# Optimization experiments

Measured on AMD Instinct MI355X. Metric: run time of the kernel, lower is better.

The kernel has to match this reference:

```python
import jax, jax.numpy as jnp
import numpy as np
from jax import lax


def _dct_basis():
    # 64 separable 2D DCT-II basis filters, shape [64,1,8,8] (OIHW)
    k = 8
    a = np.full(k, np.sqrt(2.0 / k)); a[0] = np.sqrt(1.0 / k)
    u = np.arange(k)[:, None]; xx = np.arange(k)[None, :]
    B = a[:, None] * np.cos((2 * xx + 1) * u * np.pi / (2 * k))  # [u, x]
    basis = np.einsum('ux,vy->uvxy', B, B).reshape(64, 1, k, k)
    return jnp.asarray(basis, dtype=jnp.float32)


def _conv(x, w, b, pad):
    y = lax.conv_general_dilated(x, w, (1, 1), [(pad, pad), (pad, pad)],
                                 dimension_numbers=('NCHW', 'OIHW', 'NCHW'))
    return y + b[None, :, None, None]


def _bn(x, s, b, m, v, eps=1e-5):
    inv = s * lax.rsqrt(v + eps)
    return x * inv[None, :, None, None] + (b - m * inv)[None, :, None, None]


def _mp2(x):
    return lax.reduce_window(x, -jnp.inf, lax.max, (1, 1, 2, 2), (1, 1, 2, 2), 'VALID')


def setup_inputs() -> dict:
    key = jax.random.key(0)
    ks = jax.random.split(key, 32)
    B = 128
    d = {}
    d['x'] = jax.random.normal(ks[0], (B, 1, 256, 256), jnp.float32)
    d['qvectors'] = jax.random.uniform(ks[1], (B, 64), jnp.float32)
    d['dct_basis'] = _dct_basis()
    def w(k, shape, sc=0.02):
        return jax.random.normal(k, shape, jnp.float32) * sc
    # conv stack
    d['conv1a_w'] = w(ks[2], (64, 1, 5, 5));   d['conv1a_b'] = w(ks[3], (64,))
    d['conv1b_w'] = w(ks[4], (64, 64, 5, 5));  d['conv1b_b'] = w(ks[5], (64,))
    d['conv2a_w'] = w(ks[6], (128, 64, 5, 5)); d['conv2a_b'] = w(ks[7], (128,))
    d['conv3a_w'] = w(ks[8], (256, 128, 5, 5)); d['conv3a_b'] = w(ks[9], (256,))
    # batchnorm (eval-mode) params: scale, bias, running_mean, running_var
    for i, (name, c) in enumerate([('bn1a', 64), ('bn1b', 64), ('bn2a', 128), ('bn3a', 256)]):
        kk = jax.random.split(ks[10 + i], 4)
        d[name + '_s'] = 1.0 + w(kk[0], (c,))
        d[name + '_b'] = w(kk[1], (c,))
        d[name + '_m'] = w(kk[2], (c,))
        d[name + '_v'] = jax.random.uniform(kk[3], (c,), jnp.float32, 0.5, 1.5)
    d['fc1_w'] = w(ks[20], (500, 15 * 8 * 256 + 64), 0.01); d['fc1_b'] = w(ks[21], (500,))
    d['fc2_w'] = w(ks[22], (500, 564), 0.01);               d['fc2_b'] = w(ks[23], (500,))
    d['fc3_w'] = w(ks[24], (2, 564), 0.01);                 d['fc3_b'] = w(ks[25], (2,))
    return d


def reference(x, qvectors, dct_basis,
              conv1a_w, conv1a_b, bn1a_s, bn1a_b, bn1a_m, bn1a_v,
              conv1b_w, conv1b_b, bn1b_s, bn1b_b, bn1b_m, bn1b_v,
              conv2a_w, conv2a_b, bn2a_s, bn2a_b, bn2a_m, bn2a_v,
              conv3a_w, conv3a_b, bn3a_s, bn3a_b, bn3a_m, bn3a_v,
              fc1_w, fc1_b, fc2_w, fc2_b, fc3_w, fc3_b):
    gamma = 1e6
    # --- soft-histogram over DCT coefficients (no_grad in the original) ---
    dct = lax.conv_general_dilated(x, dct_basis, (8, 8), 'VALID',
                                   dimension_numbers=('NCHW', 'OIHW', 'NCHW'))  # [B,64,32,32]
    bins = jnp.arange(-60, 61, dtype=jnp.float32)  # 121 bins

    def step(_, b):
        s = jnp.sum(jax.nn.sigmoid(gamma * (dct - b)), axis=(2, 3)) / 1024.0  # [B,64]
        return None, s
    _, feats = lax.scan(step, None, bins)           # [121,B,64]
    feats = jnp.transpose(feats, (1, 0, 2))          # [B,121,64]
    features = feats[:, 0:120, :] - feats[:, 1:121, :]
    features = lax.stop_gradient(features.reshape(-1, 1, 120, 64))

    # --- CNN backbone ---
    h = jax.nn.relu(_bn(_conv(features, conv1a_w, conv1a_b, 2), bn1a_s, bn1a_b, bn1a_m, bn1a_v))
    h = jax.nn.relu(_bn(_conv(h, conv1b_w, conv1b_b, 2), bn1b_s, bn1b_b, bn1b_m, bn1b_v))
    h = _mp2(h)
    h = jax.nn.relu(_bn(_conv(h, conv2a_w, conv2a_b, 2), bn2a_s, bn2a_b, bn2a_m, bn2a_v))
    h = _mp2(h)
    h = jax.nn.relu(_bn(_conv(h, conv3a_w, conv3a_b, 2), bn3a_s, bn3a_b, bn3a_m, bn3a_v))
    h = _mp2(h)                                      # [B,256,15,8]
    h_flat = h.reshape(-1, 15 * 8 * 256)
    h = jnp.concatenate([qvectors, h_flat], axis=1)
    h = jax.nn.relu(h @ fc1_w.T + fc1_b)
    h = jnp.concatenate([qvectors, h], axis=1)
    h = jax.nn.relu(h @ fc2_w.T + fc2_b)
    h = jnp.concatenate([qvectors, h], axis=1)
    return h @ fc3_w.T + fc3_b
```

## Files before the change

### kernel.cpp

```cpp
#include <hip/hip_runtime.h>


typedef _Float16 half8 __attribute__((ext_vector_type(8)));
typedef _Float16 half4 __attribute__((ext_vector_type(4)));
typedef float f32x16 __attribute__((ext_vector_type(16)));

__device__ __forceinline__ void async_copy16(const void* g, void* l) {
  __builtin_amdgcn_global_load_lds(
      (__attribute__((address_space(1))) void*)g,
      (__attribute__((address_space(3))) void*)l, 16, 0, 0);
}

__global__ __launch_bounds__(256) void dct_kernel(const float* __restrict__ x,
                                                  const float* __restrict__ basis,
                                                  float* __restrict__ dct) {
  __shared__ __align__(16) float Bm[64];
  int tid = threadIdx.x;
  if (tid < 64) {
    int u = tid >> 3, xx = tid & 7;
    Bm[tid] = basis[(u * 8) * 64 + xx * 8] * 2.8284271247461903f;
  }
  __syncthreads();
  int gid = blockIdx.x * 256 + tid;
  int b = gid >> 10, blk = gid & 1023;
  int bi = blk >> 5, bj = blk & 31;
  const float* xp = x + (size_t)b * 65536 + (bi * 8) * 256 + bj * 8;
  float X[64];
#pragma unroll
  for (int r = 0; r < 8; ++r) {
    float4 p = *(const float4*)(xp + r * 256);
    float4 q = *(const float4*)(xp + r * 256 + 4);
    X[r * 8 + 0] = p.x; X[r * 8 + 1] = p.y; X[r * 8 + 2] = p.z; X[r * 8 + 3] = p.w;
    X[r * 8 + 4] = q.x; X[r * 8 + 5] = q.y; X[r * 8 + 6] = q.z; X[r * 8 + 7] = q.w;
  }
  float T[64];
#pragma unroll
  for (int u = 0; u < 8; ++u) {
    float t[8] = {0.f, 0.f, 0.f, 0.f, 0.f, 0.f, 0.f, 0.f};
#pragma unroll
    for (int xx = 0; xx < 8; ++xx) {
      float bm = Bm[u * 8 + xx];
#pragma unroll
      for (int y = 0; y < 8; ++y) t[y] += bm * X[xx * 8 + y];
    }
#pragma unroll
    for (int y = 0; y < 8; ++y) T[u * 8 + y] = t[y];
  }
  float* op = dct + (size_t)b * 65536 + bi * 32 + bj;
#pragma unroll
  for (int v = 0; v < 8; ++v) {
    float dc[8] = {0.f, 0.f, 0.f, 0.f, 0.f, 0.f, 0.f, 0.f};
#pragma unroll
    for (int y = 0; y < 8; ++y) {
      float bm = Bm[v * 8 + y];
#pragma unroll
      for (int u = 0; u < 8; ++u) dc[u] += bm * T[u * 8 + y];
    }
#pragma unroll
    for (int u = 0; u < 8; ++u) op[(u * 8 + v) * 1024] = dc[u];
  }
}

__global__ __launch_bounds__(256) void hist_kernel(const float* __restrict__ dct,
                                                   float* __restrict__ feat) {
  __shared__ __align__(16) float h[16 * 121];
  int tid = threadIdx.x;
  for (int i = tid; i < 16 * 121; i += 256) h[i] = 0.f;
  __syncthreads();
  int b = blockIdx.x >> 6, c = blockIdx.x & 63;
  const float* dp = dct + (size_t)(b * 64 + c) * 1024;
  float* hc = h + (tid & 15) * 121;
  float4 v4 = ((const float4*)dp)[tid];
  float vals[4] = {v4.x, v4.y, v4.z, v4.w};
#pragma unroll
  for (int i = 0; i < 4; ++i) {
    float d = vals[i];
    float fl = floorf(d);
    float t0 = d - fl;
    int k = (int)fl + 60;
    if (t0 >= 2e-5f && t0 <= 1.f - 1.2e-4f) {
      if (k >= 0 && k < 120) atomicAdd(hc + k, 1.0f);
    } else {
      float s0 = 1.f / (1.f + expf(-1e6f * t0));
      float s1 = 1.f / (1.f + expf(1e6f * (1.f - t0)));
      if (k >= 1 && k <= 120) atomicAdd(hc + k - 1, 1.f - s0);
      if (k >= 0 && k < 120)  atomicAdd(hc + k, s0 - s1);
      if (k >= -1 && k < 119) atomicAdd(hc + k + 1, s1);
    }
  }
  __syncthreads();
  for (int f = tid; f < 120; f += 256) {
    float s = 0.f;
#pragma unroll
    for (int l = 0; l < 16; ++l) s += h[l * 121 + f];
    feat[((size_t)b * 120 + f) * 64 + c] = s * (1.f / 1024.f);
  }
}

template <int CI, int CO>
__global__ __launch_bounds__(256) void wtrans(const float* __restrict__ w,
                                              _Float16* __restrict__ wt) {
  int i = blockIdx.x * 256 + threadIdx.x;
  if (i >= (CI / 8) * 30 * CO * 8) return;
  int c8 = i & 7;
  int t = i >> 3;
  int co = t % CO; t /= CO;
  int k = t % 30;
  int cg = t / 30;
  int ci = cg * 8 + c8;
  int kh = k / 6, kw = k % 6;
  float v = (kw < 5) ? w[((size_t)co * CI + ci) * 25 + kh * 5 + kw] : 0.f;
  wt[i] = (_Float16)v;
}

__global__ __launch_bounds__(256) void bnprep(const float* __restrict__ cb,
                                              const float* __restrict__ s,
                                              const float* __restrict__ b,
                                              const float* __restrict__ m,
                                              const float* __restrict__ v,
                                              float* __restrict__ scale,
                                              float* __restrict__ shift, int n) {
  int i = threadIdx.x;
  if (i < n) {
    float inv = s[i] * rsqrtf(v[i] + 1e-5f);
    scale[i] = inv;
    shift[i] = (cb[i] - m[i]) * inv + b[i];
  }
}

__global__ __launch_bounds__(256) void conv1a_f16(
    const float* __restrict__ in, const float* __restrict__ wts,
    const float* __restrict__ cb, const float* __restrict__ s_,
    const float* __restrict__ b_, const float* __restrict__ m_,
    const float* __restrict__ v_, _Float16* __restrict__ out) {
  __shared__ __align__(16) float wl[5 * 8 * 20];
  __shared__ __align__(16) float il[12 * 68];
  int tid = threadIdx.x, bid = blockIdx.x;
  int img = bid / 30;
  int r = bid % 30;
  int cob = r / 15;
  int h0 = (r % 15) * 8;
  int cog = tid & 7, wg = (tid >> 3) & 3, hh = tid >> 5;
  float acc[4][16];
#pragma unroll
  for (int i = 0; i < 4; ++i)
#pragma unroll
    for (int j = 0; j < 16; ++j) acc[i][j] = 0.f;
  for (int idx = tid; idx < 32 * 25; idx += 256) {
    int rr = idx % 25, co = idx / 25;
    float v = wts[(cob * 32 + co) * 25 + rr];
    int kh = rr / 5, kw = rr % 5;
    wl[(kh * 8 + (co >> 2)) * 20 + (co & 3) * 5 + kw] = v;
  }
  for (int idx = tid; idx < 12 * 68; idx += 256) {
    int cc = idx % 68, rr = idx / 68;
    int hy = h0 + rr - 2, wx = cc - 2;
    float v = 0.f;
    if (hy >= 0 && hy < 120 && wx >= 0 && wx < 64)
      v = in[(size_t)img * 7680 + hy * 64 + wx];
    il[idx] = v;
  }
  __syncthreads();
#pragma unroll
  for (int kh = 0; kh < 5; ++kh) {
    const float* ir = &il[(hh + kh) * 68 + wg * 16];
    float iv[20];
#pragma unroll
    for (int i = 0; i < 5; ++i) {
      float4 p = *(const float4*)(ir + i * 4);
      iv[i * 4] = p.x; iv[i * 4 + 1] = p.y; iv[i * 4 + 2] = p.z; iv[i * 4 + 3] = p.w;
    }
    const float* wr = &wl[(kh * 8 + cog) * 20];
    float wv[20];
#pragma unroll
    for (int i = 0; i < 5; ++i) {
      float4 p = *(const float4*)(wr + i * 4);
      wv[i * 4] = p.x; wv[i * 4 + 1] = p.y; wv[i * 4 + 2] = p.z; wv[i * 4 + 3] = p.w;
    }
#pragma unroll
    for (int co = 0; co < 4; ++co)
#pragma unroll
      for (int kw = 0; kw < 5; ++kw) {
        float w1 = wv[co * 5 + kw];
#pragma unroll
        for (int w = 0; w < 16; ++w) acc[co][w] += w1 * iv[w + kw];
      }
  }
  int h = h0 + hh;
  int co0 = cob * 32 + cog * 4;
  float inv[4], bia[4];
#pragma unroll
  for (int i = 0; i < 4; ++i) {
    int c = co0 + i;
    inv[i] = s_[c] * rsqrtf(v_[c] + 1e-5f);
    bia[i] = (cb[c] - m_[c]) * inv[i] + b_[c];
  }
  int g = co0 >> 3, off = co0 & 7;
  _Float16* op = out + (((size_t)(img * 8 + g) * 120 + h) * 64) * 8 + off;
#pragma unroll
  for (int w = 0; w < 16; ++w) {
    half4 o;
#pragma unroll
    for (int i = 0; i < 4; ++i)
      o[i] = (_Float16)fmaxf(acc[i][w] * inv[i] + bia[i], 0.f);
    *(half4*)&op[(size_t)(wg * 16 + w) * 8] = o;
  }
}

template <int CI, int CO, int H, int W, int BLK_M, bool OUT_NCHW>
__global__ __launch_bounds__(256, 2) void conv5_mfma(
    const _Float16* __restrict__ in, const _Float16* __restrict__ wt,
    const float* __restrict__ scale, const float* __restrict__ shift,
    _Float16* __restrict__ out) {
  constexpr int NW_M = BLK_M / 64;
  constexpr int NW_N = 4 / NW_M;
  constexpr int BLK_N = NW_N * 128;
  constexpr int ROWS = BLK_N / W;
  constexpr int TB = (H + ROWS - 1) / ROWS;
  constexpr int NCOB = CO / BLK_M;
  constexpr int HR = ROWS + 4;
  constexpr int HC = W + 4;
  constexpr int CIG = CI / 8;
  constexpr int AITER = (HR * HC + 255) / 256;
  constexpr int WBYTES = 30 * BLK_M * 16;
  constexpr int WITER = (WBYTES + 4095) / 4096;
  __shared__ __align__(16) _Float16 Alds[HR * HC * 8 + 8];
  __shared__ __align__(16) _Float16 Wlds[30 * BLK_M * 8];

  int tid = threadIdx.x;
  int bid = blockIdx.x;
  int img = bid / (TB * NCOB);
  int r = bid % (TB * NCOB);
  int tb = r / NCOB;
  int cob = r % NCOB;
  int h0 = tb * ROWS;

  int wid = tid >> 6, l = tid & 63, lo = l & 31, hi = l >> 5;
  int widM = wid / NW_N, widN = wid % NW_N;

  if (tid < 8) Alds[HR * HC * 8 + tid] = (_Float16)0.f;

  int wbase[2];
#pragma unroll
  for (int mi = 0; mi < 2; ++mi)
    wbase[mi] = (hi * BLK_M + widM * 64 + mi * 32 + lo) * 8;
  int bbase[4], pr_[4], pc_[4];
#pragma unroll
  for (int j = 0; j < 4; ++j) {
    int pix = widN * 128 + j * 32 + lo;
    pr_[j] = pix / W;
    pc_[j] = pix % W;
    bbase[j] = (pr_[j] * HC + pc_[j] + hi) * 8;
  }

  f32x16 acc[2][4];
#pragma unroll
  for (int mi = 0; mi < 2; ++mi)
#pragma unroll
    for (int j = 0; j < 4; ++j) acc[mi][j] = (f32x16){};

#pragma unroll 1
  for (int ci0 = 0; ci0 < CI; ci0 += 8) {
    int cg = ci0 >> 3;
    const _Float16* ing = in + (size_t)(img * CIG + cg) * H * W * 8;
    half8 areg[AITER];
#pragma unroll
    for (int it = 0; it < AITER; ++it) {
      int i = tid + it * 256;
      half8 v = {};
      if (i < HR * HC) {
        int rr = i / HC, cc = i % HC;
        int hy = h0 + rr - 2, wx = cc - 2;
        if (hy >= 0 && hy < H && wx >= 0 && wx < W)
          v = *(const half8*)&ing[(size_t)(hy * W + wx) * 8];
      }
      areg[it] = v;
    }
    const char* wsrc = (const char*)(wt + ((size_t)cg * 30 * CO + cob * BLK_M) * 8);
#pragma unroll
    for (int rr = 0; rr < WITER; ++rr) {
      int f = rr * 4096 + tid * 16;
      if (f < WBYTES) {
        int row = f / (BLK_M * 16);
        int off = f % (BLK_M * 16);
        async_copy16(wsrc + (size_t)row * (CO * 16) + off,
                     (char*)Wlds + (rr * 4096 + wid * 1024));
      }
    }
#pragma unroll
    for (int it = 0; it < AITER; ++it) {
      int i = tid + it * 256;
      if (i < HR * HC) *(half8*)&Alds[i * 8] = areg[it];
    }
    __syncthreads();
#pragma unroll
    for (int kh = 0; kh < 5; ++kh) {
#pragma unroll
      for (int kwb = 0; kwb < 3; ++kwb) {
        half8 af[2], bf[4];
#pragma unroll
        for (int mi = 0; mi < 2; ++mi)
          af[mi] = *(const half8*)&Wlds[wbase[mi] + (kh * 6 + 2 * kwb) * BLK_M * 8];
#pragma unroll
        for (int j = 0; j < 4; ++j)
          bf[j] = *(const half8*)&Alds[bbase[j] + (kh * HC + 2 * kwb) * 8];
#pragma unroll
        for (int mi = 0; mi < 2; ++mi)
#pragma unroll
          for (int j = 0; j < 4; ++j)
            acc[mi][j] = __builtin_amdgcn_mfma_f32_32x32x16_f16(
                af[mi], bf[j], acc[mi][j], 0, 0, 0);
      }
    }
    __syncthreads();
  }

  if (!OUT_NCHW) {
    constexpr int CGO = CO / 8;
    int gbase = (cob * BLK_M + widM * 64) >> 3;
#pragma unroll
    for (int mi = 0; mi < 2; ++mi) {
#pragma unroll
      for (int r4 = 0; r4 < 4; ++r4) {
        int g = gbase + mi * 4 + r4;
        int co0 = g * 8 + hi * 4;
        float4 sv = *(const float4*)&scale[co0];
        float4 tv = *(const float4*)&shift[co0];
#pragma unroll
        for (int j = 0; j < 4; ++j) {
          int hy = h0 + pr_[j];
          if (hy < H) {
            half4 o;
            o[0] = (_Float16)fmaxf(acc[mi][j][r4 * 4 + 0] * sv.x + tv.x, 0.f);
            o[1] = (_Float16)fmaxf(acc[mi][j][r4 * 4 + 1] * sv.y + tv.y, 0.f);
            o[2] = (_Float16)fmaxf(acc[mi][j][r4 * 4 + 2] * sv.z + tv.z, 0.f);
            o[3] = (_Float16)fmaxf(acc[mi][j][r4 * 4 + 3] * sv.w + tv.w, 0.f);
            *(half4*)&out[(((size_t)(img * CGO + g) * H + hy) * W + pc_[j]) * 8 +
                          hi * 4] = o;
          }
        }
      }
    }
  } else {
#pragma unroll
    for (int mi = 0; mi < 2; ++mi) {
#pragma unroll
      for (int reg = 0; reg < 16; ++reg) {
        int co = cob * BLK_M + widM * 64 + mi * 32 + (reg & 3) + 8 * (reg >> 2) + 4 * hi;
        float s = scale[co], t = shift[co];
#pragma unroll
        for (int j = 0; j < 4; ++j) {
          int hy = h0 + pr_[j];
          if (hy < H)
            out[((size_t)(img * CO + co) * H + hy) * W + pc_[j]] =
                (_Float16)fmaxf(acc[mi][j][reg] * s + t, 0.f);
        }
      }
    }
  }
}

template <int IMGS, int CG, int H, int W>
__global__ __launch_bounds__(256) void pool_g(const _Float16* __restrict__ in,
                                              _Float16* __restrict__ out) {
  constexpr int OH = H / 2, OW = W / 2;
  int idx = blockIdx.x * 256 + threadIdx.x;
  constexpr int TOTAL = IMGS * CG * OH * OW;
  if (idx >= TOTAL) return;
  int ow = idx % OW;
  int t = idx / OW;
  int oh = t % OH; t /= OH;
  int g = t % CG;
  int img = t / CG;
  const half8* in8 = (const half8*)in;
  size_t base = ((size_t)(img * CG + g) * H + 2 * oh) * W + 2 * ow;
  half8 a = in8[base], b = in8[base + 1], c = in8[base + W], d = in8[base + W + 1];
  half8 o;
#pragma unroll
  for (int i = 0; i < 8; ++i) {
    _Float16 m0 = a[i] > b[i] ? a[i] : b[i];
    _Float16 m1 = c[i] > d[i] ? c[i] : d[i];
    o[i] = m0 > m1 ? m0 : m1;
  }
  ((half8*)out)[((size_t)(img * CG + g) * OH + oh) * OW + ow] = o;
}

__global__ __launch_bounds__(256) void pool_nchw(const _Float16* __restrict__ in,
                                                 _Float16* __restrict__ out) {
  int idx = blockIdx.x * 256 + threadIdx.x;
  if (idx >= 128 * 256 * 15) return;
  int oh = idx % 15;
  int t = idx / 15;
  int c = t % 256;
  int img = t / 256;
  const half8* r = (const half8*)(in + ((size_t)(img * 256 + c) * 30 + 2 * oh) * 16);
  half8 x0 = r[0], x1 = r[1], y0 = r[2], y1 = r[3];
  half8 o;
#pragma unroll
  for (int ow = 0; ow < 4; ++ow) {
    _Float16 m0 = x0[2 * ow] > x0[2 * ow + 1] ? x0[2 * ow] : x0[2 * ow + 1];
    _Float16 m1 = y0[2 * ow] > y0[2 * ow + 1] ? y0[2 * ow] : y0[2 * ow + 1];
    o[ow] = m0 > m1 ? m0 : m1;
    _Float16 n0 = x1[2 * ow] > x1[2 * ow + 1] ? x1[2 * ow] : x1[2 * ow + 1];
    _Float16 n1 = y1[2 * ow] > y1[2 * ow + 1] ? y1[2 * ow] : y1[2 * ow + 1];
    o[ow + 4] = n0 > n1 ? n0 : n1;
  }
  ((half8*)out)[((size_t)(img * 256 + c) * 15 + oh)] = o;
}

__global__ __launch_bounds__(256, 2) void fc1_mfma(const float* __restrict__ qv,
                                                   const _Float16* __restrict__ p3,
                                                   const float* __restrict__ w,
                                                   float* __restrict__ part) {
  __shared__ __align__(16) _Float16 Wl[8 * 256 * 8];
  __shared__ __align__(16) _Float16 Bl[8 * 128 * 8];
  int tid = threadIdx.x;
  int ks = blockIdx.x >> 1, mt = blockIdx.x & 1;
  int wid = tid >> 6, l = tid & 63, lo = l & 31, hi = l >> 5;
  f32x16 acc[2][4];
#pragma unroll
  for (int mi = 0; mi < 2; ++mi)
#pragma unroll
    for (int j = 0; j < 4; ++j) acc[mi][j] = (f32x16){};

#pragma unroll 1
  for (int i3 = 0; i3 < 3; ++i3) {
    int c = ks + 240 * i3;
    if (c > 480) break;
    for (int idx = tid; idx < 2048; idx += 256) {
      int n_loc = idx >> 3, k8 = idx & 7;
      int n = mt * 256 + n_loc;
      half8 v = {};
      if (n < 500) {
        const float* src = w + (size_t)n * 30784 + c * 64 + k8 * 8;
        float4 f0 = *(const float4*)src;
        float4 f1 = *(const float4*)(src + 4);
        v[0] = (_Float16)f0.x; v[1] = (_Float16)f0.y;
        v[2] = (_Float16)f0.z; v[3] = (_Float16)f0.w;
        v[4] = (_Float16)f1.x; v[5] = (_Float16)f1.y;
        v[6] = (_Float16)f1.z; v[7] = (_Float16)f1.w;
      }
      *(half8*)&Wl[(size_t)(k8 * 256 + n_loc) * 8] = v;
    }
    for (int idx = tid; idx < 1024; idx += 256) {
      int img = idx >> 3, k8 = idx & 7;
      half8 v;
      if (c == 0) {
        const float* src = qv + img * 64 + k8 * 8;
        float4 f0 = *(const float4*)src;
        float4 f1 = *(const float4*)(src + 4);
        v[0] = (_Float16)f0.x; v[1] = (_Float16)f0.y;
        v[2] = (_Float16)f0.z; v[3] = (_Float16)f0.w;
        v[4] = (_Float16)f1.x; v[5] = (_Float16)f1.y;
        v[6] = (_Float16)f1.z; v[7] = (_Float16)f1.w;
      } else {
        v = *(const half8*)&p3[(size_t)img * 30720 + (c * 64 - 64) + k8 * 8];
      }
      *(half8*)&Bl[(size_t)(k8 * 128 + img) * 8] = v;
    }
    __syncthreads();
#pragma unroll
    for (int ks16 = 0; ks16 < 4; ++ks16) {
      half8 af[2], bf[4];
#pragma unroll
      for (int mi = 0; mi < 2; ++mi)
        af[mi] = *(const half8*)&Wl[(size_t)((ks16 * 2 + hi) * 256 + wid * 64 +
                                             mi * 32 + lo) * 8];
#pragma unroll
      for (int j = 0; j < 4; ++j)
        bf[j] = *(const half8*)&Bl[(size_t)((ks16 * 2 + hi) * 128 + j * 32 + lo) * 8];
#pragma unroll
      for (int mi = 0; mi < 2; ++mi)
#pragma unroll
        for (int j = 0; j < 4; ++j)
          acc[mi][j] = __builtin_amdgcn_mfma_f32_32x32x16_f16(
              af[mi], bf[j], acc[mi][j], 0, 0, 0);
    }
    __syncthreads();
  }
#pragma unroll
  for (int mi = 0; mi < 2; ++mi)
#pragma unroll
    for (int reg = 0; reg < 16; ++reg) {
      int n = mt * 256 + wid * 64 + mi * 32 + (reg & 3) + 8 * (reg >> 2) + 4 * hi;
#pragma unroll
      for (int j = 0; j < 4; ++j)
        part[((size_t)ks * 512 + n) * 128 + j * 32 + lo] = acc[mi][j][reg];
    }
}

__global__ __launch_bounds__(256) void fc1_reduce(const float* __restrict__ part,
                                                  const float* __restrict__ bias,
                                                  float* __restrict__ out) {
  int idx = blockIdx.x * 256 + threadIdx.x;
  int img = idx & 127, n = idx >> 7;
  float s = 0.f;
#pragma unroll 8
  for (int ks = 0; ks < 240; ++ks) s += part[((size_t)ks * 512 + n) * 128 + img];
  out[n * 128 + img] = (n < 500) ? fmaxf(s + bias[n], 0.f) : 0.f;
}

__global__ __launch_bounds__(256) void fc2_kernel(const float* __restrict__ qv,
                                                  const float* __restrict__ fc1o,
                                                  const float* __restrict__ w,
                                                  const float* __restrict__ bias,
                                                  float* __restrict__ out) {
  int idx = blockIdx.x * 256 + threadIdx.x;
  if (idx >= 128 * 500) return;
  int m = idx & 127, n = idx >> 7;
  const float* wr = w + (size_t)n * 564;
  float acc = 0.f;
#pragma unroll 8
  for (int k = 0; k < 64; ++k) acc += qv[m * 64 + k] * wr[k];
#pragma unroll 4
  for (int k = 0; k < 500; ++k) acc += fc1o[k * 128 + m] * wr[64 + k];
  out[n * 128 + m] = fmaxf(acc + bias[n], 0.f);
}

__global__ __launch_bounds__(256) void fc3_kernel(const float* __restrict__ qv,
                                                  const float* __restrict__ fc2o,
                                                  const float* __restrict__ w,
                                                  const float* __restrict__ bias,
                                                  float* __restrict__ out) {
  int tid = threadIdx.x;
  int m = tid >> 1, n = tid & 1;
  const float* wr = w + (size_t)n * 564;
  float acc = 0.f;
#pragma unroll 8
  for (int k = 0; k < 64; ++k) acc += qv[m * 64 + k] * wr[k];
#pragma unroll 4
  for (int k = 0; k < 500; ++k) acc += fc2o[k * 128 + m] * wr[64 + k];
  out[m * 2 + n] = acc + bias[n];
}

extern "C" void kernel_launch(void* const* d_in, const int* in_sizes, int n_in,
                              void* d_out, int out_size, void* d_ws, size_t ws_size,
                              hipStream_t stream) {
  (void)in_sizes; (void)n_in; (void)out_size; (void)ws_size;
  const float* x      = (const float*)d_in[0];
  const float* qv     = (const float*)d_in[1];
  const float* basis  = (const float*)d_in[2];
  const float* c1aw   = (const float*)d_in[3];
  const float* c1ab   = (const float*)d_in[4];
  const float* c1bw   = (const float*)d_in[5];
  const float* c1bb   = (const float*)d_in[6];
  const float* c2aw   = (const float*)d_in[7];
  const float* c2ab   = (const float*)d_in[8];
  const float* c3aw   = (const float*)d_in[9];
  const float* c3ab   = (const float*)d_in[10];
  const float* bn1a_s = (const float*)d_in[11];
  const float* bn1a_b = (const float*)d_in[12];
  const float* bn1a_m = (const float*)d_in[13];
  const float* bn1a_v = (const float*)d_in[14];
  const float* bn1b_s = (const float*)d_in[15];
  const float* bn1b_b = (const float*)d_in[16];
  const float* bn1b_m = (const float*)d_in[17];
  const float* bn1b_v = (const float*)d_in[18];
  const float* bn2a_s = (const float*)d_in[19];
  const float* bn2a_b = (const float*)d_in[20];
  const float* bn2a_m = (const float*)d_in[21];
  const float* bn2a_v = (const float*)d_in[22];
  const float* bn3a_s = (const float*)d_in[23];
  const float* bn3a_b = (const float*)d_in[24];
  const float* bn3a_m = (const float*)d_in[25];
  const float* bn3a_v = (const float*)d_in[26];
  const float* fc1w   = (const float*)d_in[27];
  const float* fc1b   = (const float*)d_in[28];
  const float* fc2w   = (const float*)d_in[29];
  const float* fc2b   = (const float*)d_in[30];
  const float* fc3w   = (const float*)d_in[31];
  const float* fc3b   = (const float*)d_in[32];

  float* ws = (float*)d_ws;
  float* feat = ws;
  _Float16* wt1b = (_Float16*)(ws + 1000000);
  _Float16* wt2a = (_Float16*)(ws + 1070000);
  _Float16* wt3a = (_Float16*)(ws + 1200000);
  float* sc1b = ws + 1700000; float* sh1b = ws + 1700100;
  float* sc2a = ws + 1700200; float* sh2a = ws + 1700400;
  float* sc3a = ws + 1700600; float* sh3a = ws + 1701000;
  _Float16* p1 = (_Float16*)(ws + 1710000);
  float* S = ws + 9600000;
  float* dct     = S;
  _Float16* a1c  = (_Float16*)S;
  _Float16* a2c  = (_Float16*)(S + 8000000);
  _Float16* a3   = (_Float16*)S;
  _Float16* p2   = (_Float16*)(S + 15750000);
  _Float16* a4   = (_Float16*)S;
  _Float16* p3   = (_Float16*)(ws + 1710000);
  float* f1p  = S;
  float* f1o  = ws + 25400000;
  float* f2o  = ws + 25500000;

  wtrans<64, 64><<<480, 256, 0, stream>>>(c1bw, wt1b);
  wtrans<64, 128><<<960, 256, 0, stream>>>(c2aw, wt2a);
  wtrans<128, 256><<<3840, 256, 0, stream>>>(c3aw, wt3a);
  bnprep<<<1, 256, 0, stream>>>(c1bb, bn1b_s, bn1b_b, bn1b_m, bn1b_v, sc1b, sh1b, 64);
  bnprep<<<1, 256, 0, stream>>>(c2ab, bn2a_s, bn2a_b, bn2a_m, bn2a_v, sc2a, sh2a, 128);
  bnprep<<<1, 256, 0, stream>>>(c3ab, bn3a_s, bn3a_b, bn3a_m, bn3a_v, sc3a, sh3a, 256);

  dct_kernel<<<512, 256, 0, stream>>>(x, basis, dct);
  hist_kernel<<<128 * 64, 256, 0, stream>>>(dct, feat);

  for (int c = 0; c < 4; ++c) {
    const float* fin = feat + (size_t)c * 32 * 120 * 64;
    _Float16* pout = p1 + (size_t)c * 32 * 8 * 60 * 32 * 8;
    conv1a_f16<<<32 * 30, 256, 0, stream>>>(fin, c1aw, c1ab, bn1a_s, bn1a_b,
                                            bn1a_m, bn1a_v, a1c);
    conv5_mfma<64, 64, 120, 64, 64, false><<<32 * 15, 256, 0, stream>>>(
        a1c, wt1b, sc1b, sh1b, a2c);
    pool_g<32, 8, 120, 64><<<1920, 256, 0, stream>>>(a2c, pout);
  }

  conv5_mfma<64, 128, 60, 32, 128, false><<<128 * 8, 256, 0, stream>>>(
      p1, wt2a, sc2a, sh2a, a3);
  pool_g<128, 16, 60, 32><<<3840, 256, 0, stream>>>(a3, p2);

  conv5_mfma<128, 256, 30, 16, 128, true><<<128 * 2 * 2, 256, 0, stream>>>(
      p2, wt3a, sc3a, sh3a, a4);
  pool_nchw<<<1920, 256, 0, stream>>>(a4, p3);

  fc1_mfma<<<480, 256, 0, stream>>>(qv, p3, fc1w, f1p);
  fc1_reduce<<<256, 256, 0, stream>>>(f1p, fc1b, f1o);
  fc2_kernel<<<250, 256, 0, stream>>>(qv, f1o, fc2w, fc2b, f2o);
  fc3_kernel<<<1, 256, 0, stream>>>(qv, f2o, fc3w, fc3b, (float*)d_out);
}
```

Baseline: 866.0 us.

## Fuse 2x2 max-pool into conv epilogues and double conv block size

Each conv5_mfma kernel now does the 2x2 max-pool in its epilogue, using lane shuffles and the accumulator layout, and writes pooled output directly. This removes the separate pool_g and pool_nchw kernels and the full-resolution activation round trip through memory. Blocks grow to 512 threads (8 waves), which doubles the output tile per block, halves the grid counts, and cuts the conv1 chunk loop from 4 to 2. The larger blocks may lower occupancy, since launch bounds no longer ask for 2 blocks per CU, and the pooling correctness depends on how tile rows and lanes are laid out.

```diff
diff --git a/kernel.cpp b/kernel.cpp
--- a/kernel.cpp
+++ b/kernel.cpp
@@ -208,12 +208,12 @@
 }
 
 template <int CI, int CO, int H, int W, int BLK_M, bool OUT_NCHW>
-__global__ __launch_bounds__(256, 2) void conv5_mfma(
+__global__ __launch_bounds__(512) void conv5_mfma(
     const _Float16* __restrict__ in, const _Float16* __restrict__ wt,
     const float* __restrict__ scale, const float* __restrict__ shift,
     _Float16* __restrict__ out) {
   constexpr int NW_M = BLK_M / 64;
-  constexpr int NW_N = 4 / NW_M;
+  constexpr int NW_N = 8 / NW_M;
   constexpr int BLK_N = NW_N * 128;
   constexpr int ROWS = BLK_N / W;
   constexpr int TB = (H + ROWS - 1) / ROWS;
@@ -221,9 +221,10 @@
   constexpr int HR = ROWS + 4;
   constexpr int HC = W + 4;
   constexpr int CIG = CI / 8;
-  constexpr int AITER = (HR * HC + 255) / 256;
+  constexpr int OH = H / 2, OW = W / 2;
+  constexpr int AITER = (HR * HC + 511) / 512;
   constexpr int WBYTES = 30 * BLK_M * 16;
-  constexpr int WITER = (WBYTES + 4095) / 4096;
+  constexpr int WITER = (WBYTES + 8191) / 8192;
   __shared__ __align__(16) _Float16 Alds[HR * HC * 8 + 8];
   __shared__ __align__(16) _Float16 Wlds[30 * BLK_M * 8];
 
@@ -244,13 +245,11 @@
 #pragma unroll
   for (int mi = 0; mi < 2; ++mi)
     wbase[mi] = (hi * BLK_M + widM * 64 + mi * 32 + lo) * 8;
-  int bbase[4], pr_[4], pc_[4];
+  int bbase[4];
 #pragma unroll
   for (int j = 0; j < 4; ++j) {
     int pix = widN * 128 + j * 32 + lo;
-    pr_[j] = pix / W;
-    pc_[j] = pix % W;
-    bbase[j] = (pr_[j] * HC + pc_[j] + hi) * 8;
+    bbase[j] = ((pix / W) * HC + (pix % W) + hi) * 8;
   }
 
   f32x16 acc[2][4];
@@ -266,7 +265,7 @@
     half8 areg[AITER];
 #pragma unroll
     for (int it = 0; it < AITER; ++it) {
-      int i = tid + it * 256;
+      int i = tid + it * 512;
       half8 v = {};
       if (i < HR * HC) {
         int rr = i / HC, cc = i % HC;
@@ -279,17 +278,17 @@
     const char* wsrc = (const char*)(wt + ((size_t)cg * 30 * CO + cob * BLK_M) * 8);
 #pragma unroll
     for (int rr = 0; rr < WITER; ++rr) {
-      int f = rr * 4096 + tid * 16;
+      int f = rr * 8192 + tid * 16;
       if (f < WBYTES) {
         int row = f / (BLK_M * 16);
         int off = f % (BLK_M * 16);
         async_copy16(wsrc + (size_t)row * (CO * 16) + off,
-                     (char*)Wlds + (rr * 4096 + wid * 1024));
+                     (char*)Wlds + (rr * 8192 + wid * 1024));
       }
     }
 #pragma unroll
     for (int it = 0; it < AITER; ++it) {
-      int i = tid + it * 256;
+      int i = tid + it * 512;
       if (i < HR * HC) *(half8*)&Alds[i * 8] = areg[it];
     }
     __syncthreads();
@@ -318,6 +317,7 @@
   if (!OUT_NCHW) {
     constexpr int CGO = CO / 8;
     int gbase = (cob * BLK_M + widM * 64) >> 3;
+    bool lane_ok = ((lo & 1) == 0);
 #pragma unroll
     for (int mi = 0; mi < 2; ++mi) {
 #pragma unroll
@@ -326,22 +326,32 @@
         int co0 = g * 8 + hi * 4;
         float4 sv = *(const float4*)&scale[co0];
         float4 tv = *(const float4*)&shift[co0];
-#pragma unroll
-        for (int j = 0; j < 4; ++j) {
-          int hy = h0 + pr_[j];
-          if (hy < H) {
-            half4 o;
-            o[0] = (_Float16)fmaxf(acc[mi][j][r4 * 4 + 0] * sv.x + tv.x, 0.f);
-            o[1] = (_Float16)fmaxf(acc[mi][j][r4 * 4 + 1] * sv.y + tv.y, 0.f);
-            o[2] = (_Float16)fmaxf(acc[mi][j][r4 * 4 + 2] * sv.z + tv.z, 0.f);
-            o[3] = (_Float16)fmaxf(acc[mi][j][r4 * 4 + 3] * sv.w + tv.w, 0.f);
-            *(half4*)&out[(((size_t)(img * CGO + g) * H + hy) * W + pc_[j]) * 8 +
+        float sa[4] = {sv.x, sv.y, sv.z, sv.w};
+        float ta[4] = {tv.x, tv.y, tv.z, tv.w};
+#pragma unroll
+        for (int p = 0; p < 2; ++p) {
+          int ja = (W == 64) ? p : 2 * p;
+          int jb = (W == 64) ? p + 2 : 2 * p + 1;
+          int orow = (W == 64) ? (h0 >> 1) + widN : (h0 >> 1) + widN * 2 + p;
+          int ocol = (W == 64) ? p * 16 + (lo >> 1) : (lo >> 1);
+          half4 o;
+#pragma unroll
+          for (int c = 0; c < 4; ++c) {
+            int reg = r4 * 4 + c;
+            float v0 = fmaxf(acc[mi][ja][reg] * sa[c] + ta[c], 0.f);
+            float v1 = fmaxf(acc[mi][jb][reg] * sa[c] + ta[c], 0.f);
+            float m = fmaxf(v0, v1);
+            m = fmaxf(m, __shfl_xor(m, 1, 64));
+            o[c] = (_Float16)m;
+          }
+          if (lane_ok && orow < OH)
+            *(half4*)&out[(((size_t)(img * CGO + g) * OH + orow) * OW + ocol) * 8 +
                           hi * 4] = o;
-          }
         }
       }
     }
   } else {
+    bool lane_ok = ((lo & 1) == 0) && (lo < 16);
 #pragma unroll
     for (int mi = 0; mi < 2; ++mi) {
 #pragma unroll
@@ -350,62 +360,17 @@
         float s = scale[co], t = shift[co];
 #pragma unroll
         for (int j = 0; j < 4; ++j) {
-          int hy = h0 + pr_[j];
-          if (hy < H)
-            out[((size_t)(img * CO + co) * H + hy) * W + pc_[j]] =
-                (_Float16)fmaxf(acc[mi][j][reg] * s + t, 0.f);
+          float v = fmaxf(acc[mi][j][reg] * s + t, 0.f);
+          float m = fmaxf(v, __shfl_xor(v, 16, 64));
+          m = fmaxf(m, __shfl_xor(m, 1, 64));
+          int orow = (h0 >> 1) + widN * 4 + j;
+          if (lane_ok && orow < OH)
+            out[((size_t)(img * CO + co) * OH + orow) * OW + ((lo & 15) >> 1)] =
+                (_Float16)m;
         }
       }
     }
   }
-}
-
-template <int IMGS, int CG, int H, int W>
-__global__ __launch_bounds__(256) void pool_g(const _Float16* __restrict__ in,
-                                              _Float16* __restrict__ out) {
-  constexpr int OH = H / 2, OW = W / 2;
-  int idx = blockIdx.x * 256 + threadIdx.x;
-  constexpr int TOTAL = IMGS * CG * OH * OW;
-  if (idx >= TOTAL) return;
-  int ow = idx % OW;
-  int t = idx / OW;
-  int oh = t % OH; t /= OH;
-  int g = t % CG;
-  int img = t / CG;
-  const half8* in8 = (const half8*)in;
-  size_t base = ((size_t)(img * CG + g) * H + 2 * oh) * W + 2 * ow;
-  half8 a = in8[base], b = in8[base + 1], c = in8[base + W], d = in8[base + W + 1];
-  half8 o;
-#pragma unroll
-  for (int i = 0; i < 8; ++i) {
-    _Float16 m0 = a[i] > b[i] ? a[i] : b[i];
-    _Float16 m1 = c[i] > d[i] ? c[i] : d[i];
-    o[i] = m0 > m1 ? m0 : m1;
-  }
-  ((half8*)out)[((size_t)(img * CG + g) * OH + oh) * OW + ow] = o;
-}
-
-__global__ __launch_bounds__(256) void pool_nchw(const _Float16* __restrict__ in,
-                                                 _Float16* __restrict__ out) {
-  int idx = blockIdx.x * 256 + threadIdx.x;
-  if (idx >= 128 * 256 * 15) return;
-  int oh = idx % 15;
-  int t = idx / 15;
-  int c = t % 256;
-  int img = t / 256;
-  const half8* r = (const half8*)(in + ((size_t)(img * 256 + c) * 30 + 2 * oh) * 16);
-  half8 x0 = r[0], x1 = r[1], y0 = r[2], y1 = r[3];
-  half8 o;
-#pragma unroll
-  for (int ow = 0; ow < 4; ++ow) {
-    _Float16 m0 = x0[2 * ow] > x0[2 * ow + 1] ? x0[2 * ow] : x0[2 * ow + 1];
-    _Float16 m1 = y0[2 * ow] > y0[2 * ow + 1] ? y0[2 * ow] : y0[2 * ow + 1];
-    o[ow] = m0 > m1 ? m0 : m1;
-    _Float16 n0 = x1[2 * ow] > x1[2 * ow + 1] ? x1[2 * ow] : x1[2 * ow + 1];
-    _Float16 n1 = y1[2 * ow] > y1[2 * ow + 1] ? y1[2 * ow] : y1[2 * ow + 1];
-    o[ow + 4] = n0 > n1 ? n0 : n1;
-  }
-  ((half8*)out)[((size_t)(img * 256 + c) * 15 + oh)] = o;
 }
 
 __global__ __launch_bounds__(256, 2) void fc1_mfma(const float* __restrict__ qv,
@@ -583,14 +548,11 @@
   float* S = ws + 9600000;
   float* dct     = S;
   _Float16* a1c  = (_Float16*)S;
-  _Float16* a2c  = (_Float16*)(S + 8000000);
-  _Float16* a3   = (_Float16*)S;
-  _Float16* p2   = (_Float16*)(S + 15750000);
-  _Float16* a4   = (_Float16*)S;
+  _Float16* p2   = (_Float16*)(ws + 25400000);
   _Float16* p3   = (_Float16*)(ws + 1710000);
   float* f1p  = S;
-  float* f1o  = ws + 25400000;
-  float* f2o  = ws + 25500000;
+  float* f1o  = ws + 29400000;
+  float* f2o  = ws + 29500000;
 
   wtrans<64, 64><<<480, 256, 0, stream>>>(c1bw, wt1b);
   wtrans<64, 128><<<960, 256, 0, stream>>>(c2aw, wt2a);
@@ -602,23 +564,20 @@
   dct_kernel<<<512, 256, 0, stream>>>(x, basis, dct);
   hist_kernel<<<128 * 64, 256, 0, stream>>>(dct, feat);
 
-  for (int c = 0; c < 4; ++c) {
-    const float* fin = feat + (size_t)c * 32 * 120 * 64;
-    _Float16* pout = p1 + (size_t)c * 32 * 8 * 60 * 32 * 8;
-    conv1a_f16<<<32 * 30, 256, 0, stream>>>(fin, c1aw, c1ab, bn1a_s, bn1a_b,
+  for (int c = 0; c < 2; ++c) {
+    const float* fin = feat + (size_t)c * 64 * 120 * 64;
+    _Float16* pout = p1 + (size_t)c * 64 * 8 * 60 * 32 * 8;
+    conv1a_f16<<<64 * 30, 256, 0, stream>>>(fin, c1aw, c1ab, bn1a_s, bn1a_b,
                                             bn1a_m, bn1a_v, a1c);
-    conv5_mfma<64, 64, 120, 64, 64, false><<<32 * 15, 256, 0, stream>>>(
-        a1c, wt1b, sc1b, sh1b, a2c);
-    pool_g<32, 8, 120, 64><<<1920, 256, 0, stream>>>(a2c, pout);
-  }
-
-  conv5_mfma<64, 128, 60, 32, 128, false><<<128 * 8, 256, 0, stream>>>(
-      p1, wt2a, sc2a, sh2a, a3);
-  pool_g<128, 16, 60, 32><<<3840, 256, 0, stream>>>(a3, p2);
-
-  conv5_mfma<128, 256, 30, 16, 128, true><<<128 * 2 * 2, 256, 0, stream>>>(
-      p2, wt3a, sc3a, sh3a, a4);
-  pool_nchw<<<1920, 256, 0, stream>>>(a4, p3);
+    conv5_mfma<64, 64, 120, 64, 64, false><<<64 * 8, 512, 0, stream>>>(
+        a1c, wt1b, sc1b, sh1b, pout);
+  }
+
+  conv5_mfma<64, 128, 60, 32, 128, false><<<128 * 4, 512, 0, stream>>>(
+      p1, wt2a, sc2a, sh2a, p2);
+
+  conv5_mfma<128, 256, 30, 16, 128, true><<<128 * 2, 512, 0, stream>>>(
+      p2, wt3a, sc3a, sh3a, p3);
 
   fc1_mfma<<<480, 256, 0, stream>>>(qv, p3, fc1w, f1p);
   fc1_reduce<<<256, 256, 0, stream>>>(f1p, fc1b, f1o);
```

Result: faster. 811.3 us (-6.3%).
